# Optimization experiments

Measured on AMD Instinct MI355X. Metric: run time of the kernel, lower is better.

Reference implementation:

```python
import jax, jax.numpy as jnp
import numpy as np

SYNC_COST = 10.0
T_START_MS, T_END_MS = 0, 500
EPS = 1e-7
_bs = np.logspace(-3, 0, 20)
BIN_MS = [int(np.round(b * 1000)) for b in _bs[_bs < (0.5 - 0.0) / 2]]  # 16 static bin widths in ms


def setup_inputs() -> dict:
    key = jax.random.key(0)
    k1, k2 = jax.random.split(key, 2)
    n_trials, T_total, n_neurons = 8, 600, 30000
    n_e, n_samples, max_count = 25000, 50, 200
    spikes = (jax.random.uniform(k1, (n_trials, T_total, n_neurons)) < 0.02).astype(jnp.float32)
    experimental_fanos_mean = jax.random.uniform(k2, (len(BIN_MS),), jnp.float32) * 2.0 + 0.5
    rng = np.random.default_rng(0)
    sample_trials = jnp.asarray(rng.integers(0, n_trials, n_samples), jnp.int32)
    # counts ~ clip(N(70,30), 15, max_count), as in the original sampling logic
    counts = np.clip(rng.normal(70, 30, n_samples).astype(np.int64), 15, max_count)
    sample_ids = jnp.asarray(rng.integers(0, n_e, (n_samples, max_count)), jnp.int64)
    sample_mask = jnp.asarray(np.arange(max_count)[None, :] < counts[:, None], jnp.float32)
    return {"spikes": spikes, "experimental_fanos_mean": experimental_fanos_mean,
            "sample_trials": sample_trials, "sample_ids": sample_ids, "sample_mask": sample_mask}


def _pop_fano(x):
    # x: [T, S] population spike-count time series per sample
    T = x.shape[0]
    fanos = []
    for bs in BIN_MS:  # static, small loop over 16 bin widths
        nb = T // bs
        counts = x[: nb * bs].reshape(nb, bs, -1).sum(axis=1)  # [nb, S]
        mean = jnp.maximum(counts.mean(axis=0), EPS)
        fanos.append(jnp.var(counts, axis=0) / mean)  # ddof=0, like tf.math.reduce_variance
    return jnp.stack(fanos)  # [n_bins, S]


def reference(spikes, experimental_fanos_mean, sample_trials, sample_ids, sample_mask):
    sp = spikes[:, T_START_MS:T_END_MS, :]  # [n_trials, T, N]

    def gather_sum(trial, ids, m):
        g = jnp.take(jnp.take(sp, trial, axis=0), ids, axis=1)  # [T, C]
        return jnp.sum(g * m[None, :], axis=-1)                 # [T]

    sel = jax.vmap(gather_sum)(sample_trials, sample_ids, sample_mask)  # [S, T]
    fanos = _pop_fano(sel.T)          # [n_bins, S]
    fanos_mean = fanos.mean(axis=1)   # [n_bins]
    mse = jnp.mean(jnp.square(experimental_fanos_mean - fanos_mean))
    return SYNC_COST * mse
```

## Files before the change

kernel.cpp:

```cpp
#include <hip/hip_runtime.h>
#include <hip/hip_bf16.h>

#define N_TRIALS   8
#define T_TOTAL    600
#define N_NEURONS  30000
#define T_USE      500
#define N_SAMPLES  50
#define MAX_COUNT  200
#define N_BINS     16
#define GROUP      8
#define EPS_D      1e-7

__device__ __constant__ int BIN_SIZES[N_BINS] = {1,1,2,3,4,6,9,13,18,26,38,55,78,113,162,234};

__global__ __launch_bounds__(256) void cnt_kernel(
    const float* __restrict__ mask, int* __restrict__ cnts)
{
    int w    = (blockIdx.x * 256 + threadIdx.x) >> 6;
    int lane = threadIdx.x & 63;
    if (w >= N_SAMPLES) return;
    const float* m = mask + w * MAX_COUNT;
    float sum = 0.f;
    for (int j = lane; j < MAX_COUNT; j += 64) sum += m[j];
    for (int k = 32; k; k >>= 1) sum += __shfl_xor(sum, k);
    if (lane == 0) cnts[w] = (int)(sum + 0.5f);
}

__global__ __launch_bounds__(256) void sel_kernel(
    const float* __restrict__ spikes,
    const int*   __restrict__ trials,
    const int*   __restrict__ ids,
    const int*   __restrict__ cnts,
    float*       __restrict__ sel)
{
    int u = blockIdx.x * 256 + threadIdx.x;
    int g = u & (GROUP - 1);
    int v = u >> 3;
    if (v >= N_SAMPLES * T_USE) return;
    int t = v % T_USE;
    int s = v / T_USE;

    int trial = trials[s];
    int cnt   = cnts[s];
    const float* row = spikes + (size_t)trial * (T_TOTAL * N_NEURONS)
                              + (size_t)t * N_NEURONS;
    const int*   sid = ids + s * MAX_COUNT;

    float acc = 0.f;
    for (int j = g; j < cnt; j += GROUP)
        acc += row[sid[j]];

    acc += __shfl_xor(acc, 1);
    acc += __shfl_xor(acc, 2);
    acc += __shfl_xor(acc, 4);
    if (g == 0) sel[v] = acc;
}

__global__ __launch_bounds__(256) void fano_stage(
    const float* __restrict__ sel,
    float*       __restrict__ fano)
{
    int w    = (blockIdx.x * 256 + threadIdx.x) >> 6;
    int lane = threadIdx.x & 63;
    if (w >= N_BINS * N_SAMPLES) return;
    int bin = w / N_SAMPLES;
    int s   = w % N_SAMPLES;
    int bs  = BIN_SIZES[bin];
    int nb  = T_USE / bs;
    const float* rowp = sel + s * T_USE;

    double sum = 0.0, sumsq = 0.0;
    for (int b = lane; b < nb; b += 64) {
        double c = 0.0;
        int base = b * bs;
        for (int q = 0; q < bs; ++q) c += (double)rowp[base + q];
        sum   += c;
        sumsq += c * c;
    }
    for (int k = 32; k; k >>= 1) {
        sum   += __shfl_xor(sum,   k);
        sumsq += __shfl_xor(sumsq, k);
    }
    if (lane == 0) {
        double mean = sum / nb;
        double var  = sumsq / nb - mean * mean;
        double m2   = mean < EPS_D ? EPS_D : mean;
        fano[w] = (float)(var / m2);
    }
}

__global__ void final_kernel(
    const float* __restrict__ fano,
    const float* __restrict__ expf,
    float*       __restrict__ out)
{
    int tid = threadIdx.x;
    double d2 = 0.0;
    if (tid < N_BINS) {
        double acc = 0.0;
        for (int s = 0; s < N_SAMPLES; ++s) acc += (double)fano[tid * N_SAMPLES + s];
        double fm   = acc / N_SAMPLES;
        double diff = (double)expf[tid] - fm;
        d2 = diff * diff;
    }
    for (int k = 32; k; k >>= 1) d2 += __shfl_xor(d2, k);
    if (tid == 0) out[0] = (float)(10.0 * d2 / N_BINS);
}

extern "C" void kernel_launch(void* const* d_in, const int* in_sizes, int n_in,
                              void* d_out, int out_size, void* d_ws, size_t ws_size,
                              hipStream_t stream)
{
    const float* spikes = (const float*)d_in[0];
    const float* expf   = (const float*)d_in[1];
    const int*   trials = (const int*)d_in[2];
    const int*   ids    = (const int*)d_in[3];
    const float* mask   = (const float*)d_in[4];
    float* out = (float*)d_out;

    float* sel  = (float*)d_ws;
    float* fano = sel + N_SAMPLES * T_USE;
    int*   cnts = (int*)(fano + N_BINS * N_SAMPLES);

    cnt_kernel<<<(N_SAMPLES * 64 + 255) / 256, 256, 0, stream>>>(mask, cnts);

    const int total = N_SAMPLES * T_USE * GROUP;
    sel_kernel<<<(total + 255) / 256, 256, 0, stream>>>(spikes, trials, ids, cnts, sel);

    fano_stage<<<(N_BINS * N_SAMPLES * 64 + 255) / 256, 256, 0, stream>>>(sel, fano);

    final_kernel<<<1, 64, 0, stream>>>(fano, expf, out);
}
```

Before: 685.5 us.

## Gather by trial using sorted (neuron, sample) pair lists with shared-memory accumulation

Replaces the per-(sample,time) gather with a per-(trial,time) gather. Valid (neuron id, sample) pairs are first bucketed by trial and bitonic-sorted by neuron id, so each spike row is read once per trial with ascending addresses. Per-sample sums are built with shared-memory atomics. This costs two extra small serial kernels (a single-block build and a sort), and rows are processed for every trial even when few samples use it.

```diff
diff --git a/kernel.cpp b/kernel.cpp
--- a/kernel.cpp
+++ b/kernel.cpp
@@ -8,52 +8,91 @@
 #define N_SAMPLES  50
 #define MAX_COUNT  200
 #define N_BINS     16
-#define GROUP      8
+#define MAXP       (N_SAMPLES * MAX_COUNT)
+#define SORT_MAX   8192
 #define EPS_D      1e-7
 
 __device__ __constant__ int BIN_SIZES[N_BINS] = {1,1,2,3,4,6,9,13,18,26,38,55,78,113,162,234};
 
-__global__ __launch_bounds__(256) void cnt_kernel(
-    const float* __restrict__ mask, int* __restrict__ cnts)
+__global__ __launch_bounds__(256) void build_pairs(
+    const int*   __restrict__ trials,
+    const int*   __restrict__ ids,
+    const float* __restrict__ mask,
+    unsigned*    __restrict__ pairs,
+    int*         __restrict__ npairs)
 {
-    int w    = (blockIdx.x * 256 + threadIdx.x) >> 6;
-    int lane = threadIdx.x & 63;
-    if (w >= N_SAMPLES) return;
-    const float* m = mask + w * MAX_COUNT;
-    float sum = 0.f;
-    for (int j = lane; j < MAX_COUNT; j += 64) sum += m[j];
-    for (int k = 32; k; k >>= 1) sum += __shfl_xor(sum, k);
-    if (lane == 0) cnts[w] = (int)(sum + 0.5f);
+    __shared__ int np[N_TRIALS];
+    int tid = threadIdx.x;
+    if (tid < N_TRIALS) np[tid] = 0;
+    __syncthreads();
+    for (int f = tid; f < N_SAMPLES * MAX_COUNT; f += 256) {
+        if (mask[f] != 0.f) {
+            int s  = f / MAX_COUNT;
+            int tr = trials[s];
+            int pos = atomicAdd(&np[tr], 1);
+            pairs[tr * MAXP + pos] = ((unsigned)ids[f] << 6) | (unsigned)s;
+        }
+    }
+    __syncthreads();
+    if (tid < N_TRIALS) npairs[tid] = np[tid];
 }
 
-__global__ __launch_bounds__(256) void sel_kernel(
-    const float* __restrict__ spikes,
-    const int*   __restrict__ trials,
-    const int*   __restrict__ ids,
-    const int*   __restrict__ cnts,
-    float*       __restrict__ sel)
+__global__ __launch_bounds__(256) void sort_pairs(
+    unsigned* __restrict__ pairs, const int* __restrict__ npairs)
 {
-    int u = blockIdx.x * 256 + threadIdx.x;
-    int g = u & (GROUP - 1);
-    int v = u >> 3;
-    if (v >= N_SAMPLES * T_USE) return;
-    int t = v % T_USE;
-    int s = v / T_USE;
+    __shared__ unsigned buf[SORT_MAX];
+    int tr = blockIdx.x;
+    int np = npairs[tr];
+    if (np <= 1 || np > SORT_MAX) return;
+    int m = 2; while (m < np) m <<= 1;
+    int tid = threadIdx.x;
+    unsigned* p = pairs + tr * MAXP;
+    for (int i = tid; i < m; i += 256) buf[i] = (i < np) ? p[i] : 0xFFFFFFFFu;
+    __syncthreads();
+    for (int k = 2; k <= m; k <<= 1) {
+        for (int j = k >> 1; j > 0; j >>= 1) {
+            for (int i = tid; i < m; i += 256) {
+                int ixj = i ^ j;
+                if (ixj > i) {
+                    unsigned a = buf[i], b = buf[ixj];
+                    bool up = ((i & k) == 0);
+                    if ((a > b) == up) { buf[i] = b; buf[ixj] = a; }
+                }
+            }
+            __syncthreads();
+        }
+    }
+    for (int i = tid; i < np; i += 256) p[i] = buf[i];
+}
 
-    int trial = trials[s];
-    int cnt   = cnts[s];
-    const float* row = spikes + (size_t)trial * (T_TOTAL * N_NEURONS)
-                              + (size_t)t * N_NEURONS;
-    const int*   sid = ids + s * MAX_COUNT;
+__global__ __launch_bounds__(256) void gather_kernel(
+    const float*    __restrict__ spikes,
+    const unsigned* __restrict__ pairs,
+    const int*      __restrict__ npairs,
+    const int*      __restrict__ trials,
+    float*          __restrict__ sel)
+{
+    __shared__ float acc[4][N_SAMPLES];
+    int w    = threadIdx.x >> 6;
+    int lane = threadIdx.x & 63;
+    int r  = blockIdx.x * 4 + w;
+    int tr = r / T_USE;
+    int t  = r % T_USE;
+    if (lane < N_SAMPLES) acc[w][lane] = 0.f;
+    __syncthreads();
 
-    float acc = 0.f;
-    for (int j = g; j < cnt; j += GROUP)
-        acc += row[sid[j]];
+    int np = npairs[tr];
+    const unsigned* pp  = pairs + tr * MAXP;
+    const float*    row = spikes + ((size_t)tr * T_TOTAL + t) * N_NEURONS;
+    for (int k = lane; k < np; k += 64) {
+        unsigned pr = pp[k];
+        float v = row[pr >> 6];
+        if (v != 0.f) atomicAdd(&acc[w][pr & 63], v);
+    }
+    __syncthreads();
 
-    acc += __shfl_xor(acc, 1);
-    acc += __shfl_xor(acc, 2);
-    acc += __shfl_xor(acc, 4);
-    if (g == 0) sel[v] = acc;
+    if (lane < N_SAMPLES && trials[lane] == tr)
+        sel[lane * T_USE + t] = acc[w][lane];
 }
 
 __global__ __launch_bounds__(256) void fano_stage(
@@ -118,14 +157,16 @@
     const float* mask   = (const float*)d_in[4];
     float* out = (float*)d_out;
 
-    float* sel  = (float*)d_ws;
-    float* fano = sel + N_SAMPLES * T_USE;
-    int*   cnts = (int*)(fano + N_BINS * N_SAMPLES);
+    float*    sel    = (float*)d_ws;
+    float*    fano   = sel + N_SAMPLES * T_USE;
+    unsigned* pairs  = (unsigned*)(fano + N_BINS * N_SAMPLES);
+    int*      npairs = (int*)(pairs + N_TRIALS * MAXP);
 
-    cnt_kernel<<<(N_SAMPLES * 64 + 255) / 256, 256, 0, stream>>>(mask, cnts);
+    build_pairs<<<1, 256, 0, stream>>>(trials, ids, mask, pairs, npairs);
+    sort_pairs<<<N_TRIALS, 256, 0, stream>>>(pairs, npairs);
 
-    const int total = N_SAMPLES * T_USE * GROUP;
-    sel_kernel<<<(total + 255) / 256, 256, 0, stream>>>(spikes, trials, ids, cnts, sel);
+    int rows = N_TRIALS * T_USE;
+    gather_kernel<<<rows / 4, 256, 0, stream>>>(spikes, pairs, npairs, trials, sel);
 
     fano_stage<<<(N_BINS * N_SAMPLES * 64 + 255) / 256, 256, 0, stream>>>(sel, fano);
 
```

Result: slower. 743.0 us (+8.4%).
